# Kernel tuning notes

Hardware: AMD Instinct MI355X
Metric: run time of the kernel (lower is better)

## Reference

```python
import jax, jax.numpy as jnp
import numpy as np

N = 100000      # nodes
E = 1600000     # edges (self-loops added in reference, as PyG GATConv does)
DIN = 512
DOUT = 16
H = 8           # heads (both layers)
C1 = 8          # out_channels of gat1
NEG_SLOPE = 0.2


def setup_inputs() -> dict:
    key = jax.random.key(0)
    ks = jax.random.split(key, 12)
    s = 0.05  # small init scale
    return {
        "x": jax.random.normal(ks[0], (N, DIN), jnp.float32),
        "edge_index": jax.random.randint(ks[1], (2, E), 0, N, jnp.int32),
        "W1": jax.random.normal(ks[2], (DIN, H * C1), jnp.float32) * s,
        "att_src1": jax.random.normal(ks[3], (H, C1), jnp.float32) * s,
        "att_dst1": jax.random.normal(ks[4], (H, C1), jnp.float32) * s,
        "bias1": jnp.zeros((H * C1,), jnp.float32),
        "prelu_w": jnp.float32(0.25),
        "W2": jax.random.normal(ks[5], (H * C1, H * DOUT), jnp.float32) * s,
        "att_src2": jax.random.normal(ks[6], (H, DOUT), jnp.float32) * s,
        "att_dst2": jax.random.normal(ks[7], (H, DOUT), jnp.float32) * s,
        "bias2": jnp.zeros((DOUT,), jnp.float32),
    }


def gat_layer(x, src, dst, W, a_src, a_dst, bias, heads, outc, concat):
    """PyG-style GATConv (eval mode, self-loops already in src/dst)."""
    n = x.shape[0]
    h = (x @ W).reshape(n, heads, outc)                 # [N, H, C]
    alpha_s = jnp.sum(h * a_src, axis=-1)               # [N, H]
    alpha_d = jnp.sum(h * a_dst, axis=-1)               # [N, H]
    # per-edge score, softmax grouped by destination node
    e = jax.nn.leaky_relu(alpha_s[src] + alpha_d[dst], NEG_SLOPE)   # [E', H]
    emax = jax.ops.segment_max(e, dst, num_segments=n)              # [N, H]
    ex = jnp.exp(e - emax[dst])
    denom = jax.ops.segment_sum(ex, dst, num_segments=n)            # [N, H]
    alpha = ex / denom[dst]                                         # [E', H]
    # weighted aggregation of source features
    out = jax.ops.segment_sum(h[src] * alpha[..., None], dst, num_segments=n)  # [N, H, C]
    out = out.reshape(n, heads * outc) if concat else out.mean(axis=1)
    return out + bias


def reference(x, edge_index, W1, att_src1, att_dst1, bias1, prelu_w,
              W2, att_src2, att_dst2, bias2):
    # add self-loops (PyG GATConv default add_self_loops=True)
    loops = jnp.arange(N, dtype=edge_index.dtype)
    src = jnp.concatenate([edge_index[0], loops])
    dst = jnp.concatenate([edge_index[1], loops])

    h = gat_layer(x, src, dst, W1, att_src1, att_dst1, bias1, H, C1, True)   # [N, 64]
    h = jnp.where(h >= 0, h, prelu_w * h)                                    # PReLU
    h = gat_layer(h, src, dst, W2, att_src2, att_dst2, bias2, H, DOUT, False)  # [N, DOUT]
    return jax.nn.log_softmax(h, axis=1)
```

## Files before the change

### kernel.cpp

```cpp
#include <hip/hip_runtime.h>
#include <hip/hip_bf16.h>

#define NN 100000
#define EE 1600000
#define ET (EE + NN)
#define NBK 391
#define NBLK 208
#define STAGE_CAP 5120

typedef unsigned short ushort_t;
typedef short short8 __attribute__((ext_vector_type(8)));
typedef float f32x4 __attribute__((ext_vector_type(4)));

static __device__ __forceinline__ float b2f(unsigned short u) {
    return __uint_as_float(((unsigned int)u) << 16);
}
static __device__ __forceinline__ unsigned short f2b(float f) {
    unsigned int x = __float_as_uint(f);
    return (unsigned short)((x + 0x7fffu + ((x >> 16) & 1u)) >> 16);
}

__global__ __launch_bounds__(256) void ktrans(const float* __restrict__ W1,
                                              const float* __restrict__ W2,
                                              ushort_t* __restrict__ W1T,
                                              ushort_t* __restrict__ W2T) {
    int tid = blockIdx.x * 256 + threadIdx.x;
    if (tid < 32768) {
        int k = tid >> 6, c = tid & 63;
        W1T[c * 512 + k] = f2b(W1[tid]);
    } else if (tid < 40960) {
        int t = tid - 32768;
        int k = t >> 7, c = t & 127;
        W2T[c * 64 + k] = f2b(W2[t]);
    }
}

__global__ __launch_bounds__(256) void kgemm1(const float* __restrict__ x,
                                              const ushort_t* __restrict__ w1t,
                                              ushort_t* __restrict__ h1) {
    __shared__ __align__(16) ushort_t xs[64][136];
    const int tid = threadIdx.x;
    const int wid = tid >> 6, lane = tid & 63;
    const int l15 = lane & 15, qq = lane >> 4;
    const int row0 = blockIdx.x * 64;
    f32x4 acc[4];
#pragma unroll
    for (int i = 0; i < 4; ++i) acc[i] = (f32x4)0.f;
    for (int kc = 0; kc < 4; ++kc) {
        float4 f[8];
#pragma unroll
        for (int i = 0; i < 8; ++i) {
            int f4i = tid + 256 * i;
            int rr = f4i >> 5;
            int cc = f4i & 31;
            long gr = (long)min(row0 + rr, NN - 1);
            f[i] = *(const float4*)(x + gr * 512 + kc * 128 + cc * 4);
        }
        __syncthreads();
#pragma unroll
        for (int i = 0; i < 8; ++i) {
            int f4i = tid + 256 * i;
            int rr = f4i >> 5, cc = f4i & 31;
            uint2 uu;
            uu.x = ((unsigned)f2b(f[i].y) << 16) | f2b(f[i].x);
            uu.y = ((unsigned)f2b(f[i].w) << 16) | f2b(f[i].z);
            *(uint2*)&xs[rr][cc * 4] = uu;
        }
        __syncthreads();
#pragma unroll
        for (int ks = 0; ks < 4; ++ks) {
            short8 b = *(const short8*)(w1t + (size_t)(wid * 16 + l15) * 512 + kc * 128 + ks * 32 + qq * 8);
#pragma unroll
            for (int mt = 0; mt < 4; ++mt) {
                short8 a = *(const short8*)&xs[mt * 16 + l15][ks * 32 + qq * 8];
                acc[mt] = __builtin_amdgcn_mfma_f32_16x16x32_bf16(a, b, acc[mt], 0, 0, 0);
            }
        }
    }
#pragma unroll
    for (int mt = 0; mt < 4; ++mt) {
        int node = row0 + mt * 16 + qq * 4;
#pragma unroll
        for (int rr = 0; rr < 4; ++rr) {
            if (node + rr < NN)
                h1[(size_t)(node + rr) * 64 + wid * 16 + l15] = f2b(acc[mt][rr]);
        }
    }
}

__global__ __launch_bounds__(256) void kgemm2(const ushort_t* __restrict__ hin,
                                              const ushort_t* __restrict__ w2t,
                                              ushort_t* __restrict__ h2) {
    __shared__ __align__(16) ushort_t xs[64][72];
    const int tid = threadIdx.x;
    const int wid = tid >> 6, lane = tid & 63;
    const int l15 = lane & 15, qq = lane >> 4;
    const int row0 = blockIdx.x * 64;
    const int r = tid >> 2, seg = tid & 3;
    const long grow = (long)min(row0 + r, NN - 1);
    const uint4* gp = (const uint4*)(hin + grow * 64 + seg * 16);
    uint4 v0 = gp[0], v1 = gp[1];
    uint4* lp = (uint4*)&xs[r][seg * 16];
    lp[0] = v0; lp[1] = v1;
    __syncthreads();
    f32x4 acc[4][2];
#pragma unroll
    for (int i = 0; i < 4; ++i)
#pragma unroll
        for (int j = 0; j < 2; ++j) acc[i][j] = (f32x4)0.f;
#pragma unroll
    for (int ks = 0; ks < 2; ++ks) {
        short8 a[4];
#pragma unroll
        for (int mt = 0; mt < 4; ++mt)
            a[mt] = *(const short8*)&xs[mt * 16 + l15][ks * 32 + qq * 8];
#pragma unroll
        for (int nt = 0; nt < 2; ++nt) {
            short8 b = *(const short8*)(w2t + (size_t)(wid * 32 + nt * 16 + l15) * 64 + ks * 32 + qq * 8);
#pragma unroll
            for (int mt = 0; mt < 4; ++mt)
                acc[mt][nt] = __builtin_amdgcn_mfma_f32_16x16x32_bf16(a[mt], b, acc[mt][nt], 0, 0, 0);
        }
    }
#pragma unroll
    for (int mt = 0; mt < 4; ++mt) {
        int node = row0 + mt * 16 + qq * 4;
#pragma unroll
        for (int nt = 0; nt < 2; ++nt) {
            int col = wid * 32 + nt * 16 + l15;
#pragma unroll
            for (int rr = 0; rr < 4; ++rr) {
                if (node + rr < NN)
                    h2[(size_t)(node + rr) * 128 + col] = f2b(acc[mt][nt][rr]);
            }
        }
    }
}


__global__ __launch_bounds__(256) void kbinh(const int* __restrict__ ei,
                                             int* __restrict__ bbcnt) {
    __shared__ int hist[NBK];
    const int t = threadIdx.x, blk = blockIdx.x;
    for (int i = t; i < NBK; i += 256) hist[i] = 0;
    __syncthreads();
    const int e0 = blk * 8192;
#pragma unroll
    for (int i = 0; i < 32; ++i) {
        int e = e0 + t + 256 * i;
        if (e < ET) {
            int dst = (e < EE) ? ei[EE + e] : (e - EE);
            atomicAdd(&hist[dst >> 8], 1);
        }
    }
    __syncthreads();
    for (int i = t; i < NBK; i += 256) bbcnt[blk * NBK + i] = hist[i];
}

__global__ __launch_bounds__(512) void kbscan(int* __restrict__ bbcnt,
                                              int* __restrict__ bbase) {
    __shared__ int tot[512];
    const int t = threadIdx.x;
    int total = 0;
    if (t < NBK) {
        int run = 0;
#pragma unroll 4
        for (int blk = 0; blk < NBLK; ++blk) {
            int idx = blk * NBK + t;
            int v = bbcnt[idx];
            bbcnt[idx] = run;
            run += v;
        }
        total = run;
    }
    tot[t] = total;
    __syncthreads();
    for (int off = 1; off < 512; off <<= 1) {
        int u = (t >= off) ? tot[t - off] : 0;
        __syncthreads();
        tot[t] += u;
        __syncthreads();
    }
    if (t < NBK) bbase[t] = tot[t] - total;
    if (t == 0) bbase[NBK] = ET;
}

__global__ __launch_bounds__(256) void kbinsct(const int* __restrict__ ei,
                                               const int* __restrict__ bbcnt,
                                               const int* __restrict__ bbase,
                                               unsigned* __restrict__ pairs) {
    __shared__ int cur[NBK];
    const int t = threadIdx.x, blk = blockIdx.x;
    for (int i = t; i < NBK; i += 256) cur[i] = bbase[i] + bbcnt[blk * NBK + i];
    __syncthreads();
    const int e0 = blk * 8192;
#pragma unroll
    for (int i = 0; i < 32; ++i) {
        int e = e0 + t + 256 * i;
        if (e < ET) {
            int src, dst;
            if (e < EE) { src = ei[e]; dst = ei[EE + e]; } else { src = dst = e - EE; }
            int pos = atomicAdd(&cur[dst >> 8], 1);
            pairs[pos] = (unsigned)src | ((unsigned)(dst & 255) << 17);
        }
    }
}

__global__ __launch_bounds__(256) void kscat2(const int* __restrict__ bbase,
                                              const unsigned* __restrict__ pairs,
                                              int* __restrict__ rowp,
                                              int* __restrict__ srt) {
    __shared__ int hist[256];
    __shared__ int scn[256];
    __shared__ int cur[256];
    __shared__ unsigned stage[STAGE_CAP];
    const int t = threadIdx.x, b = blockIdx.x;
    const int j0 = bbase[b], j1 = bbase[b + 1];
    const int cnt = j1 - j0;
    hist[t] = 0;
    __syncthreads();
    for (int i = t; i < cnt; i += 256) {
        unsigned p = pairs[j0 + i];
        if (i < STAGE_CAP) stage[i] = p;
        atomicAdd(&hist[p >> 17], 1);
    }
    __syncthreads();
    const int h = hist[t];
    scn[t] = h;
    __syncthreads();
    for (int off = 1; off < 256; off <<= 1) {
        int u = (t >= off) ? scn[t - off] : 0;
        __syncthreads();
        scn[t] += u;
        __syncthreads();
    }
    const int pref = scn[t] - h;
    const int node = b * 256 + t;
    if (node < NN) rowp[node] = j0 + pref;
    if (b == 0 && t == 0) rowp[NN] = ET;
    cur[t] = pref;
    __syncthreads();
    for (int i = t; i < cnt; i += 256) {
        unsigned p = (i < STAGE_CAP) ? stage[i] : pairs[j0 + i];
        int l = (int)(p >> 17);
        int pos = atomicAdd(&cur[l], 1);
        srt[j0 + pos] = (int)(p & 0x1FFFFu);
    }
}

__global__ __launch_bounds__(256) void kagg1(const int* __restrict__ rowp,
                                             const int* __restrict__ srt,
                                             const ushort_t* __restrict__ h1,
                                             const float* __restrict__ aws,
                                             const float* __restrict__ awd,
                                             const float* __restrict__ b1,
                                             const float* __restrict__ pw,
                                             ushort_t* __restrict__ hin) {
    int tid = blockIdx.x * 256 + threadIdx.x;
    int n = tid >> 3, h = tid & 7;
    float as_w[8], ad_w[8];
#pragma unroll
    for (int c = 0; c < 8; ++c) { as_w[c] = aws[h * 8 + c]; ad_w[c] = awd[h * 8 + c]; }
    uint4 hd = *(const uint4*)(h1 + (size_t)n * 64 + h * 8);
    const ushort_t* hdp = (const ushort_t*)&hd;
    float ad = 0.f;
#pragma unroll
    for (int c = 0; c < 8; ++c) ad += b2f(hdp[c]) * ad_w[c];
    int j0 = rowp[n], j1 = rowp[n + 1];
    float num[8]; float den = 0.f;
#pragma unroll
    for (int c = 0; c < 8; ++c) num[c] = 0.f;
    for (int j = j0; j < j1; ++j) {
        int s = srt[j];
        uint4 hv = *(const uint4*)(h1 + (size_t)s * 64 + h * 8);
        const ushort_t* hp = (const ushort_t*)&hv;
        float va[8];
#pragma unroll
        for (int c = 0; c < 8; ++c) va[c] = b2f(hp[c]);
        float sc = ad;
#pragma unroll
        for (int c = 0; c < 8; ++c) sc += va[c] * as_w[c];
        sc = (sc >= 0.f) ? sc : 0.2f * sc;
        float w = __expf(sc);
        den += w;
#pragma unroll
        for (int c = 0; c < 8; ++c) num[c] += w * va[c];
    }
    float inv = 1.f / den;
    float pwf = pw[0];
    ushort_t o[8];
#pragma unroll
    for (int c = 0; c < 8; ++c) {
        float v = num[c] * inv + b1[h * 8 + c];
        v = (v >= 0.f) ? v : pwf * v;
        o[c] = f2b(v);
    }
    *(uint4*)(hin + (size_t)n * 64 + h * 8) = *(uint4*)o;
}

__global__ __launch_bounds__(256) void kagg2(const int* __restrict__ rowp,
                                             const int* __restrict__ srt,
                                             const ushort_t* __restrict__ h2,
                                             const float* __restrict__ aws,
                                             const float* __restrict__ awd,
                                             const float* __restrict__ b2,
                                             float* __restrict__ out) {
    __shared__ float red[32][17];
    int t = threadIdx.x;
    int nl = t >> 3, h = t & 7;
    int n = blockIdx.x * 32 + nl;
    for (int i = t; i < 32 * 17; i += 256) ((float*)red)[i] = 0.f;
    __syncthreads();
    float as_w[16], ad_w[16];
#pragma unroll
    for (int c = 0; c < 16; ++c) { as_w[c] = aws[h * 16 + c]; ad_w[c] = awd[h * 16 + c]; }
    uint4 d0 = *(const uint4*)(h2 + (size_t)n * 128 + h * 16);
    uint4 d1 = *(const uint4*)(h2 + (size_t)n * 128 + h * 16 + 8);
    const ushort_t* dp0 = (const ushort_t*)&d0;
    const ushort_t* dp1 = (const ushort_t*)&d1;
    float ad = 0.f;
#pragma unroll
    for (int c = 0; c < 8; ++c) { ad += b2f(dp0[c]) * ad_w[c]; ad += b2f(dp1[c]) * ad_w[8 + c]; }
    int j0 = rowp[n], j1 = rowp[n + 1];
    float num[16]; float den = 0.f;
#pragma unroll
    for (int c = 0; c < 16; ++c) num[c] = 0.f;
    for (int j = j0; j < j1; ++j) {
        int s = srt[j];
        uint4 v0 = *(const uint4*)(h2 + (size_t)s * 128 + h * 16);
        uint4 v1 = *(const uint4*)(h2 + (size_t)s * 128 + h * 16 + 8);
        const ushort_t* p0 = (const ushort_t*)&v0;
        const ushort_t* p1 = (const ushort_t*)&v1;
        float va[16];
#pragma unroll
        for (int c = 0; c < 8; ++c) { va[c] = b2f(p0[c]); va[8 + c] = b2f(p1[c]); }
        float sc = ad;
#pragma unroll
        for (int c = 0; c < 16; ++c) sc += va[c] * as_w[c];
        sc = (sc >= 0.f) ? sc : 0.2f * sc;
        float w = __expf(sc);
        den += w;
#pragma unroll
        for (int c = 0; c < 16; ++c) num[c] += w * va[c];
    }
    float sden = 0.125f / den;
#pragma unroll
    for (int k = 0; k < 16; ++k) {
        int c = (h * 2 + k) & 15;
        atomicAdd(&red[nl][c], num[c] * sden);
    }
    __syncthreads();
    if (t < 32) {
        float v[16];
#pragma unroll
        for (int d = 0; d < 16; ++d) v[d] = red[t][d] + b2[d];
        float m = v[0];
#pragma unroll
        for (int d = 1; d < 16; ++d) m = fmaxf(m, v[d]);
        float sum = 0.f;
#pragma unroll
        for (int d = 0; d < 16; ++d) sum += __expf(v[d] - m);
        float ls = __logf(sum) + m;
        float* op = out + (size_t)(blockIdx.x * 32 + t) * 16;
#pragma unroll
        for (int d = 0; d < 16; ++d) op[d] = v[d] - ls;
    }
}

extern "C" void kernel_launch(void* const* d_in, const int* in_sizes, int n_in,
                              void* d_out, int out_size, void* d_ws, size_t ws_size,
                              hipStream_t stream) {
    const float* x    = (const float*)d_in[0];
    const int*   ei   = (const int*)d_in[1];
    const float* W1   = (const float*)d_in[2];
    const float* aws1 = (const float*)d_in[3];
    const float* awd1 = (const float*)d_in[4];
    const float* b1   = (const float*)d_in[5];
    const float* pw   = (const float*)d_in[6];
    const float* W2   = (const float*)d_in[7];
    const float* aws2 = (const float*)d_in[8];
    const float* awd2 = (const float*)d_in[9];
    const float* b2   = (const float*)d_in[10];
    float* out = (float*)d_out;

    char* ws = (char*)d_ws;
    int*      srt   = (int*)(ws + 0);
    int*      rowp  = (int*)(ws + 6800000);
    int*      bbcnt = (int*)(ws + 7200256);
    int*      bbase = (int*)(ws + 7600384);
    unsigned* pairs = (unsigned*)(ws + 8000000);
    ushort_t* hin   = (ushort_t*)(ws + 8000000);
    ushort_t* h1    = (ushort_t*)(ws + 20800000);
    ushort_t* h2    = (ushort_t*)(ws + 20800000);
    ushort_t* W1T   = (ushort_t*)(ws + 46400000);
    ushort_t* W2T   = (ushort_t*)(ws + 46465536);

    ktrans<<<160, 256, 0, stream>>>(W1, W2, W1T, W2T);
    kgemm1<<<1563, 256, 0, stream>>>(x, W1T, h1);
    kbinh<<<NBLK, 256, 0, stream>>>(ei, bbcnt);
    kbscan<<<1, 512, 0, stream>>>(bbcnt, bbase);
    kbinsct<<<NBLK, 256, 0, stream>>>(ei, bbcnt, bbase, pairs);
    kscat2<<<NBK, 256, 0, stream>>>(bbase, pairs, rowp, srt);
    kagg1<<<3125, 256, 0, stream>>>(rowp, srt, h1, aws1, awd1, b1, pw, hin);
    kgemm2<<<1563, 256, 0, stream>>>(hin, W2T, h2);
    kagg2<<<3125, 256, 0, stream>>>(rowp, srt, h2, aws2, awd2, b2, out);
}
```

Baseline: 583.3 us.

## Split each node's edge loop across two lanes with software-prefetched gathers

```diff
diff --git a/kernel.cpp b/kernel.cpp
--- a/kernel.cpp
+++ b/kernel.cpp
@@ -257,7 +257,9 @@
                                              const float* __restrict__ pw,
                                              ushort_t* __restrict__ hin) {
     int tid = blockIdx.x * 256 + threadIdx.x;
-    int n = tid >> 3, h = tid & 7;
+    int n = tid >> 4;
+    int sub = tid & 15;
+    int h = sub >> 1, half = sub & 1;
     float as_w[8], ad_w[8];
 #pragma unroll
     for (int c = 0; c < 8; ++c) { as_w[c] = aws[h * 8 + c]; ad_w[c] = awd[h * 8 + c]; }
@@ -270,9 +272,19 @@
     float num[8]; float den = 0.f;
 #pragma unroll
     for (int c = 0; c < 8; ++c) num[c] = 0.f;
-    for (int j = j0; j < j1; ++j) {
+    int j = j0 + half;
+    uint4 hv;
+    if (j < j1) {
         int s = srt[j];
-        uint4 hv = *(const uint4*)(h1 + (size_t)s * 64 + h * 8);
+        hv = *(const uint4*)(h1 + (size_t)s * 64 + h * 8);
+    }
+    while (j < j1) {
+        int jn = j + 2;
+        uint4 hn;
+        if (jn < j1) {
+            int sn = srt[jn];
+            hn = *(const uint4*)(h1 + (size_t)sn * 64 + h * 8);
+        }
         const ushort_t* hp = (const ushort_t*)&hv;
         float va[8];
 #pragma unroll
@@ -285,17 +297,24 @@
         den += w;
 #pragma unroll
         for (int c = 0; c < 8; ++c) num[c] += w * va[c];
-    }
-    float inv = 1.f / den;
-    float pwf = pw[0];
-    ushort_t o[8];
-#pragma unroll
-    for (int c = 0; c < 8; ++c) {
-        float v = num[c] * inv + b1[h * 8 + c];
-        v = (v >= 0.f) ? v : pwf * v;
-        o[c] = f2b(v);
-    }
-    *(uint4*)(hin + (size_t)n * 64 + h * 8) = *(uint4*)o;
+        j = jn;
+        hv = hn;
+    }
+#pragma unroll
+    for (int c = 0; c < 8; ++c) num[c] += __shfl_xor(num[c], 1);
+    den += __shfl_xor(den, 1);
+    if (half == 0) {
+        float inv = 1.f / den;
+        float pwf = pw[0];
+        ushort_t o[8];
+#pragma unroll
+        for (int c = 0; c < 8; ++c) {
+            float v = num[c] * inv + b1[h * 8 + c];
+            v = (v >= 0.f) ? v : pwf * v;
+            o[c] = f2b(v);
+        }
+        *(uint4*)(hin + (size_t)n * 64 + h * 8) = *(uint4*)o;
+    }
 }
 
 __global__ __launch_bounds__(256) void kagg2(const int* __restrict__ rowp,
@@ -305,11 +324,12 @@
                                              const float* __restrict__ awd,
                                              const float* __restrict__ b2,
                                              float* __restrict__ out) {
-    __shared__ float red[32][17];
+    __shared__ float red[16][17];
     int t = threadIdx.x;
-    int nl = t >> 3, h = t & 7;
-    int n = blockIdx.x * 32 + nl;
-    for (int i = t; i < 32 * 17; i += 256) ((float*)red)[i] = 0.f;
+    int nl = t >> 4, sub = t & 15;
+    int h = sub >> 1, half = sub & 1;
+    int n = blockIdx.x * 16 + nl;
+    for (int i = t; i < 16 * 17; i += 256) ((float*)red)[i] = 0.f;
     __syncthreads();
     float as_w[16], ad_w[16];
 #pragma unroll
@@ -325,10 +345,21 @@
     float num[16]; float den = 0.f;
 #pragma unroll
     for (int c = 0; c < 16; ++c) num[c] = 0.f;
-    for (int j = j0; j < j1; ++j) {
+    int j = j0 + half;
+    uint4 v0, v1;
+    if (j < j1) {
         int s = srt[j];
-        uint4 v0 = *(const uint4*)(h2 + (size_t)s * 128 + h * 16);
-        uint4 v1 = *(const uint4*)(h2 + (size_t)s * 128 + h * 16 + 8);
+        const uint4* rp = (const uint4*)(h2 + (size_t)s * 128 + h * 16);
+        v0 = rp[0]; v1 = rp[1];
+    }
+    while (j < j1) {
+        int jn = j + 2;
+        uint4 n0, n1;
+        if (jn < j1) {
+            int sn = srt[jn];
+            const uint4* rp = (const uint4*)(h2 + (size_t)sn * 128 + h * 16);
+            n0 = rp[0]; n1 = rp[1];
+        }
         const ushort_t* p0 = (const ushort_t*)&v0;
         const ushort_t* p1 = (const ushort_t*)&v1;
         float va[16];
@@ -342,15 +373,20 @@
         den += w;
 #pragma unroll
         for (int c = 0; c < 16; ++c) num[c] += w * va[c];
-    }
+        j = jn;
+        v0 = n0; v1 = n1;
+    }
+#pragma unroll
+    for (int c = 0; c < 16; ++c) num[c] += __shfl_xor(num[c], 1);
+    den += __shfl_xor(den, 1);
     float sden = 0.125f / den;
 #pragma unroll
-    for (int k = 0; k < 16; ++k) {
-        int c = (h * 2 + k) & 15;
+    for (int k = 0; k < 8; ++k) {
+        int c = half * 8 + ((h + k) & 7);
         atomicAdd(&red[nl][c], num[c] * sden);
     }
     __syncthreads();
-    if (t < 32) {
+    if (t < 16) {
         float v[16];
 #pragma unroll
         for (int d = 0; d < 16; ++d) v[d] = red[t][d] + b2[d];
@@ -361,7 +397,7 @@
 #pragma unroll
         for (int d = 0; d < 16; ++d) sum += __expf(v[d] - m);
         float ls = __logf(sum) + m;
-        float* op = out + (size_t)(blockIdx.x * 32 + t) * 16;
+        float* op = out + (size_t)(blockIdx.x * 16 + t) * 16;
 #pragma unroll
         for (int d = 0; d < 16; ++d) op[d] = v[d] - ls;
     }
@@ -401,7 +437,7 @@
     kbscan<<<1, 512, 0, stream>>>(bbcnt, bbase);
     kbinsct<<<NBLK, 256, 0, stream>>>(ei, bbcnt, bbase, pairs);
     kscat2<<<NBK, 256, 0, stream>>>(bbase, pairs, rowp, srt);
-    kagg1<<<3125, 256, 0, stream>>>(rowp, srt, h1, aws1, awd1, b1, pw, hin);
+    kagg1<<<6250, 256, 0, stream>>>(rowp, srt, h1, aws1, awd1, b1, pw, hin);
     kgemm2<<<1563, 256, 0, stream>>>(hin, W2T, h2);
-    kagg2<<<3125, 256, 0, stream>>>(rowp, srt, h2, aws2, awd2, b2, out);
-}
+    kagg2<<<6250, 256, 0, stream>>>(rowp, srt, h2, aws2, awd2, b2, out);
+}
```

Measured after the change: 575.4 us. No clear change (-1.4%).
